# Kernel tuning notes

Hardware: AMD Instinct MI355X
Metric: run time of the kernel (lower is better)

The kernel has to match this reference:

```python
import jax, jax.numpy as jnp
import numpy as np

B, S, E, H, D = 2, 4096, 512, 8, 64  # batch, seq, embed, heads, key_dim


def setup_inputs() -> dict:
    key = jax.random.key(0)
    ks = jax.random.split(key, 8)
    queries = jax.random.normal(ks[0], (B, S, E), dtype=jnp.float32)
    keys = jax.random.normal(ks[1], (B, S, E), dtype=jnp.float32)
    values = jax.random.normal(ks[2], (B, S, E), dtype=jnp.float32)
    mask = jax.random.randint(ks[3], (B, H, S, S), 0, 2).astype(bool)
    scale = 1.0 / np.sqrt(E)
    Wq = jax.random.normal(ks[4], (E, H * D), dtype=jnp.float32) * scale
    Wk = jax.random.normal(ks[5], (E, H * D), dtype=jnp.float32) * scale
    Wv = jax.random.normal(ks[6], (E, H * D), dtype=jnp.float32) * scale
    Wo = jax.random.normal(ks[7], (H * D, E), dtype=jnp.float32) * scale
    return {"queries": queries, "keys": keys, "values": values, "mask": mask,
            "Wq": Wq, "Wk": Wk, "Wv": Wv, "Wo": Wo}


def reference(queries, keys, values, mask, Wq, Wk, Wv, Wo):
    # QKV projections (no bias), reshape to heads: (B, S, H, D)
    q = (queries @ Wq).reshape(B, -1, H, D)
    k = (keys @ Wk).reshape(B, -1, H, D)
    v = (values @ Wv).reshape(B, -1, H, D)
    # scores: (B, H, Sq, Sk)
    scores = jnp.einsum("bqhd,bkhd->bhqk", q, k) / jnp.sqrt(jnp.float32(D))
    scores = jnp.where(mask, jnp.float32(-1e10), scores)
    attn = jax.nn.softmax(scores, axis=-1)
    out = jnp.einsum("bhqk,bkhd->bqhd", attn, v).reshape(B, -1, H * D)
    return out @ Wo
```

## Files before the change

kernel.cpp:

```cpp
#include <hip/hip_runtime.h>
#include <hip/hip_bf16.h>

#define NB 2
#define NS 4096
#define NE 512
#define NH 8
#define ND 64
#define NHD 512

typedef __attribute__((ext_vector_type(8))) short short8;
typedef __attribute__((ext_vector_type(4))) float floatx4;
typedef __attribute__((ext_vector_type(16))) float f32x16;

#define MFMA16(a, b, c) __builtin_amdgcn_mfma_f32_16x16x32_bf16((a), (b), (c), 0, 0, 0)
#define MFMA32(a, b, c) __builtin_amdgcn_mfma_f32_32x32x16_bf16((a), (b), (c), 0, 0, 0)

union Cvt8 { uint4 u; short8 s; };
static __device__ __forceinline__ short8 ld8(const __hip_bfloat16* p) {
  Cvt8 c; c.u = *(const uint4*)p; return c.s;
}
union BH { __hip_bfloat16 h; short s; };
static __device__ __forceinline__ short f2bs(float x) {
  BH u; u.h = __float2bfloat16(x); return u.s;
}
static __device__ __forceinline__ unsigned pk2(float a, float b) {
  unsigned d;
  asm("v_cvt_pk_bf16_f32 %0, %1, %2" : "=v"(d) : "v"(a), "v"(b));
  return d;
}
static __device__ __forceinline__ float fexp2(float x) {
  float r;
  asm("v_exp_f32 %0, %1" : "=v"(r) : "v"(x));
  return r;
}

__global__ __launch_bounds__(256) void wconv(
    const float* w0, const float* w1, const float* w2, const float* w3,
    __hip_bfloat16* t0, __hip_bfloat16* t1,
    __hip_bfloat16* t2, __hip_bfloat16* t3) {
  __shared__ __hip_bfloat16 tile[64][72];
  const float* src;
  __hip_bfloat16* dst;
  switch (blockIdx.z) {
    case 0: src = w0; dst = t0; break;
    case 1: src = w1; dst = t1; break;
    case 2: src = w2; dst = t2; break;
    default: src = w3; dst = t3; break;
  }
  const int tx = threadIdx.x & 63, ty = threadIdx.x >> 6;
  const int n0 = blockIdx.x * 64, k0 = blockIdx.y * 64;
  for (int r = ty; r < 64; r += 4)
    tile[r][tx] = __float2bfloat16(src[(long)(k0 + r) * 512 + n0 + tx]);
  __syncthreads();
  for (int r = ty; r < 64; r += 4)
    dst[(long)(n0 + r) * 512 + k0 + tx] = tile[tx][r];
}

__global__ __launch_bounds__(256) void gemm_qkv(
    const float* A0, const float* A1, const float* A2,
    const __hip_bfloat16* W0, const __hip_bfloat16* W1, const __hip_bfloat16* W2,
    __hip_bfloat16* O0, __hip_bfloat16* O1, __hip_bfloat16* O2) {
  const float* A;
  const __hip_bfloat16* Wt;
  __hip_bfloat16* O;
  switch (blockIdx.z) {
    case 0: A = A0; Wt = W0; O = O0; break;
    case 1: A = A1; Wt = W1; O = O1; break;
    default: A = A2; Wt = W2; O = O2; break;
  }
  const int lane = threadIdx.x & 63;
  const int w = threadIdx.x >> 6;
  const int c = lane & 15, g = lane >> 4;
  const int m0 = blockIdx.x * 64 + w * 16;
  const int n0 = blockIdx.y * 64;

  floatx4 acc[4] = {};
  const float* ap = A + (long)(m0 + c) * 512 + g * 8;
  const __hip_bfloat16* wp = Wt + (long)(n0 + c) * 512 + g * 8;
  for (int ks = 0; ks < 512; ks += 32) {
    const float4 f0 = *(const float4*)(ap + ks);
    const float4 f1 = *(const float4*)(ap + ks + 4);
    short8 a;
    a[0] = f2bs(f0.x); a[1] = f2bs(f0.y); a[2] = f2bs(f0.z); a[3] = f2bs(f0.w);
    a[4] = f2bs(f1.x); a[5] = f2bs(f1.y); a[6] = f2bs(f1.z); a[7] = f2bs(f1.w);
#pragma unroll
    for (int t = 0; t < 4; ++t) {
      short8 b = ld8(wp + t * 16 * 512 + ks);
      acc[t] = MFMA16(a, b, acc[t]);
    }
  }
  const float sc = (blockIdx.z == 0) ? 0.125f * 1.44269504f : 1.0f;
#pragma unroll
  for (int t = 0; t < 4; ++t) {
#pragma unroll
    for (int r = 0; r < 4; ++r) {
      const int m = m0 + g * 4 + r;
      const int n = n0 + t * 16 + c;
      const int bb = m >> 12, s = m & 4095, h = n >> 6, d = n & 63;
      O[(((long)bb * NH + h) * NS + s) * ND + d] = __float2bfloat16(acc[t][r] * sc);
    }
  }
}

#define VPAD 72
__device__ __forceinline__ int vswz(int row) { return ((row >> 3) & 7) * 8; }

__global__ __launch_bounds__(256) void flash_attn(
    const __hip_bfloat16* Q, const __hip_bfloat16* K, const __hip_bfloat16* V,
    const int* __restrict__ mask, __hip_bfloat16* AO) {
  __shared__ __hip_bfloat16 Ks[64 * VPAD];
  __shared__ __hip_bfloat16 Vt[64 * VPAD];

  const int tid = threadIdx.x;
  const int lane = tid & 63, w = tid >> 6;
  const int ql = lane & 31, hl = lane >> 5;
  const int bz = blockIdx.z, hy = blockIdx.y;
  const int q0 = blockIdx.x * 128 + w * 32;
  const long headbase = ((long)bz * NH + hy) * NS;

  short8 qf[4];
#pragma unroll
  for (int ds = 0; ds < 4; ++ds)
    qf[ds] = ld8(Q + (headbase + q0 + ql) * ND + ds * 16 + hl * 8);

  f32x16 oacc0 = {}, oacc1 = {};
  float m_i = -1e30f, l_i = 0.f;
  const int* mrow = mask + (headbase + q0 + ql) * (long)NS;

  for (int kt = 0; kt < 64; ++kt) {
    const int k0 = kt * 64;

    int4 mk0, mk1, mk2, mk3, mk4, mk5, mk6, mk7;
    {
      const int* mp = mrow + k0 + 4 * hl;
      mk0 = *(const int4*)(mp + 0);
      mk1 = *(const int4*)(mp + 8);
      mk2 = *(const int4*)(mp + 16);
      mk3 = *(const int4*)(mp + 24);
      mk4 = *(const int4*)(mp + 32);
      mk5 = *(const int4*)(mp + 40);
      mk6 = *(const int4*)(mp + 48);
      mk7 = *(const int4*)(mp + 56);
    }

#pragma unroll
    for (int it = 0; it < 2; ++it) {
      const int chunk = tid + it * 256;
      const int kc = chunk >> 3;
      const int dd = (chunk & 7) * 8;
      const long gbase = (headbase + k0 + kc) * ND + dd;
      *(uint4*)&Ks[kc * VPAD + dd] = *(const uint4*)(K + gbase);
      uint4 vv = *(const uint4*)(V + gbase);
      const __hip_bfloat16* ve = (const __hip_bfloat16*)&vv;
#pragma unroll
      for (int j = 0; j < 8; ++j) {
        const int row = dd + j;
        Vt[row * VPAD + (kc ^ vswz(row))] = ve[j];
      }
    }
    __syncthreads();

    f32x16 s0 = {}, s1 = {};
#pragma unroll
    for (int ds = 0; ds < 4; ++ds) {
      short8 a0 = ld8(&Ks[ql * VPAD + ds * 16 + hl * 8]);
      s0 = MFMA32(a0, qf[ds], s0);
      short8 a1 = ld8(&Ks[(32 + ql) * VPAD + ds * 16 + hl * 8]);
      s1 = MFMA32(a1, qf[ds], s1);
    }

#pragma unroll
    for (int rr = 0; rr < 4; ++rr) {
      int4 a, b;
      switch (rr) {
        case 0: a = mk0; b = mk4; break;
        case 1: a = mk1; b = mk5; break;
        case 2: a = mk2; b = mk6; break;
        default: a = mk3; b = mk7; break;
      }
      if (a.x != 0) s0[4 * rr + 0] = -1e10f;
      if (a.y != 0) s0[4 * rr + 1] = -1e10f;
      if (a.z != 0) s0[4 * rr + 2] = -1e10f;
      if (a.w != 0) s0[4 * rr + 3] = -1e10f;
      if (b.x != 0) s1[4 * rr + 0] = -1e10f;
      if (b.y != 0) s1[4 * rr + 1] = -1e10f;
      if (b.z != 0) s1[4 * rr + 2] = -1e10f;
      if (b.w != 0) s1[4 * rr + 3] = -1e10f;
    }

    float mt = -1e30f;
#pragma unroll
    for (int r = 0; r < 16; ++r)
      mt = fmaxf(mt, fmaxf(s0[r], s1[r]));
    mt = fmaxf(mt, __shfl_xor(mt, 32));

    if (__ballot(mt > m_i + 8.0f) != 0ull) {
      const float mn = fmaxf(m_i, mt);
      const float al = fexp2(m_i - mn);
      m_i = mn;
      l_i *= al;
#pragma unroll
      for (int r = 0; r < 16; ++r) {
        const float ab = __shfl(al, (r & 3) + 8 * (r >> 2) + 4 * hl);
        oacc0[r] *= ab;
        oacc1[r] *= ab;
      }
    }

    float ss = 0.f;
#pragma unroll
    for (int r = 0; r < 16; ++r) {
      const float p0 = fexp2(s0[r] - m_i);
      const float p1 = fexp2(s1[r] - m_i);
      s0[r] = p0; s1[r] = p1;
      ss += p0 + p1;
    }
    ss += __shfl_xor(ss, 32);
    l_i += ss;

#pragma unroll
    for (int ks = 0; ks < 4; ++ks) {
      float pp[8];
#pragma unroll
      for (int j = 0; j < 8; ++j)
        pp[j] = (ks < 2) ? ((ks & 1) ? s0[8 + j] : s0[j])
                         : ((ks & 1) ? s1[8 + j] : s1[j]);
      const unsigned pk01 = pk2(pp[0], pp[1]);
      const unsigned pk23 = pk2(pp[2], pp[3]);
      const unsigned pk45 = pk2(pp[4], pp[5]);
      const unsigned pk67 = pk2(pp[6], pp[7]);
      const unsigned send1 = hl ? pk01 : pk45;
      const unsigned send2 = hl ? pk23 : pk67;
      const unsigned recv1 = __shfl_xor(send1, 32);
      const unsigned recv2 = __shfl_xor(send2, 32);
      Cvt8 pc;
      pc.u = make_uint4(hl ? recv1 : pk01,
                        hl ? recv2 : pk23,
                        hl ? pk45 : recv1,
                        hl ? pk67 : recv2);
      const int cb = ks * 16 + hl * 8;
      const short8 v0 = ld8(&Vt[ql * VPAD + (cb ^ vswz(ql))]);
      oacc0 = MFMA32(pc.s, v0, oacc0);
      const short8 v1 = ld8(&Vt[(32 + ql) * VPAD + (cb ^ vswz(32 + ql))]);
      oacc1 = MFMA32(pc.s, v1, oacc1);
    }
    __syncthreads();
  }

#pragma unroll
  for (int r = 0; r < 16; ++r) {
    const int cr = (r & 3) + 8 * (r >> 2) + 4 * hl;
    const float lb = __shfl(l_i, cr);
    const float inv = 1.0f / lb;
    const long obase = ((long)bz * NS + q0 + cr) * NHD + hy * 64;
    AO[obase + ql] = __float2bfloat16(oacc0[r] * inv);
    AO[obase + 32 + ql] = __float2bfloat16(oacc1[r] * inv);
  }
}

__global__ __launch_bounds__(256) void gemm_out(
    const __hip_bfloat16* A, const __hip_bfloat16* Wt, float* O) {
  const int lane = threadIdx.x & 63;
  const int w = threadIdx.x >> 6;
  const int c = lane & 15, g = lane >> 4;
  const int m0 = blockIdx.x * 64 + w * 16;
  const int n0 = blockIdx.y * 64;

  floatx4 acc[4] = {};
  const __hip_bfloat16* ap = A + (long)(m0 + c) * 512 + g * 8;
  const __hip_bfloat16* wp = Wt + (long)(n0 + c) * 512 + g * 8;
  for (int ks = 0; ks < 512; ks += 32) {
    short8 a = ld8(ap + ks);
#pragma unroll
    for (int t = 0; t < 4; ++t) {
      short8 b = ld8(wp + t * 16 * 512 + ks);
      acc[t] = MFMA16(a, b, acc[t]);
    }
  }
#pragma unroll
  for (int t = 0; t < 4; ++t)
#pragma unroll
    for (int r = 0; r < 4; ++r)
      O[(long)(m0 + g * 4 + r) * 512 + n0 + t * 16 + c] = acc[t][r];
}

extern "C" void kernel_launch(void* const* d_in, const int* in_sizes, int n_in,
                              void* d_out, int out_size, void* d_ws, size_t ws_size,
                              hipStream_t stream) {
  const float* q_in = (const float*)d_in[0];
  const float* k_in = (const float*)d_in[1];
  const float* v_in = (const float*)d_in[2];
  const int* mask = (const int*)d_in[3];
  const float* Wq = (const float*)d_in[4];
  const float* Wk = (const float*)d_in[5];
  const float* Wv = (const float*)d_in[6];
  const float* Wo = (const float*)d_in[7];
  float* out = (float*)d_out;

  char* base = (char*)d_ws;
  const size_t MB = 1u << 20;
  __hip_bfloat16* wtq = (__hip_bfloat16*)(base);
  __hip_bfloat16* wtk = (__hip_bfloat16*)(base + 512 * 1024);
  __hip_bfloat16* wtv = (__hip_bfloat16*)(base + 1 * MB);
  __hip_bfloat16* wto = (__hip_bfloat16*)(base + 1 * MB + 512 * 1024);
  __hip_bfloat16* qp = (__hip_bfloat16*)(base + 2 * MB);
  __hip_bfloat16* kp = (__hip_bfloat16*)(base + 10 * MB);
  __hip_bfloat16* vp = (__hip_bfloat16*)(base + 18 * MB);
  __hip_bfloat16* ao = (__hip_bfloat16*)(base + 26 * MB);

  wconv<<<dim3(8, 8, 4), 256, 0, stream>>>(Wq, Wk, Wv, Wo, wtq, wtk, wtv, wto);
  gemm_qkv<<<dim3(128, 8, 3), 256, 0, stream>>>(
      q_in, k_in, v_in, wtq, wtk, wtv, qp, kp, vp);
  flash_attn<<<dim3(NS / 128, NH, NB), 256, 0, stream>>>(qp, kp, vp, mask, ao);
  gemm_out<<<dim3(128, 8), 256, 0, stream>>>(ao, wto, out);
}
```

Before: 1.610 ms.

## Double-buffer K/V tiles with register prefetch and remap blocks across XCDs

Double-buffers the K and transposed-V tiles in shared memory. The next tile's global loads are issued into registers before this tile's compute and written to the other buffer afterwards, so one barrier per iteration remains and load latency is hidden behind the MFMAs. The mask is read with nontemporal loads, MFMA sections get raised wave priority, and the block index is remapped so blocks sharing a head land on the same XCD for L2 reuse. Costs are twice the LDS and more live registers, which may lower occupancy.

After: 1.689 ms. 4.9% more time.

```diff
diff --git a/kernel.cpp b/kernel.cpp
--- a/kernel.cpp
+++ b/kernel.cpp
@@ -11,6 +11,7 @@
 typedef __attribute__((ext_vector_type(8))) short short8;
 typedef __attribute__((ext_vector_type(4))) float floatx4;
 typedef __attribute__((ext_vector_type(16))) float f32x16;
+typedef __attribute__((ext_vector_type(4))) int intx4;
 
 #define MFMA16(a, b, c) __builtin_amdgcn_mfma_f32_16x16x32_bf16((a), (b), (c), 0, 0, 0)
 #define MFMA32(a, b, c) __builtin_amdgcn_mfma_f32_32x32x16_bf16((a), (b), (c), 0, 0, 0)
@@ -105,18 +106,52 @@
 #define VPAD 72
 __device__ __forceinline__ int vswz(int row) { return ((row >> 3) & 7) * 8; }
 
+#define STAGE_LOAD(kt_)                                                      \
+  do {                                                                       \
+    const long gb0 = (headbase + (kt_) * 64 + kc) * (long)ND + dd;           \
+    const long gb1 = gb0 + 32 * ND;                                          \
+    k0r = *(const uint4*)(K + gb0);                                          \
+    v0r = *(const uint4*)(V + gb0);                                          \
+    k1r = *(const uint4*)(K + gb1);                                          \
+    v1r = *(const uint4*)(V + gb1);                                          \
+  } while (0)
+
+#define STAGE_WRITE(buf_)                                                    \
+  do {                                                                       \
+    *(uint4*)&Ks[buf_][kc * VPAD + dd] = k0r;                                \
+    *(uint4*)&Ks[buf_][(kc + 32) * VPAD + dd] = k1r;                         \
+    const __hip_bfloat16* ve0 = (const __hip_bfloat16*)&v0r;                 \
+    const __hip_bfloat16* ve1 = (const __hip_bfloat16*)&v1r;                 \
+    _Pragma("unroll")                                                        \
+    for (int jj = 0; jj < 8; ++jj) {                                         \
+      const int row = dd + jj;                                               \
+      Vt[buf_][row * VPAD + (kc ^ vswz(row))] = ve0[jj];                     \
+      Vt[buf_][row * VPAD + ((kc + 32) ^ vswz(row))] = ve1[jj];              \
+    }                                                                        \
+  } while (0)
+
 __global__ __launch_bounds__(256) void flash_attn(
     const __hip_bfloat16* Q, const __hip_bfloat16* K, const __hip_bfloat16* V,
     const int* __restrict__ mask, __hip_bfloat16* AO) {
-  __shared__ __hip_bfloat16 Ks[64 * VPAD];
-  __shared__ __hip_bfloat16 Vt[64 * VPAD];
+  __shared__ __hip_bfloat16 Ks[2][64 * VPAD];
+  __shared__ __hip_bfloat16 Vt[2][64 * VPAD];
 
   const int tid = threadIdx.x;
   const int lane = tid & 63, w = tid >> 6;
   const int ql = lane & 31, hl = lane >> 5;
-  const int bz = blockIdx.z, hy = blockIdx.y;
-  const int q0 = blockIdx.x * 128 + w * 32;
+
+  const int L = blockIdx.x + 32 * (blockIdx.y + 8 * blockIdx.z);
+  const int cxcd = L & 7, j = L >> 3;
+  const int h2 = cxcd + 8 * (j >> 5);
+  const int bx = j & 31;
+  const int hy = h2 & 7, bz = h2 >> 3;
+
+  const int q0 = bx * 128 + w * 32;
   const long headbase = ((long)bz * NH + hy) * NS;
+
+  const int kc = tid >> 3;
+  const int dd = (tid & 7) * 8;
+  uint4 k0r, k1r, v0r, v1r;
 
   short8 qf[4];
 #pragma unroll
@@ -127,65 +162,45 @@
   float m_i = -1e30f, l_i = 0.f;
   const int* mrow = mask + (headbase + q0 + ql) * (long)NS;
 
+  STAGE_LOAD(0);
+  STAGE_WRITE(0);
+  __syncthreads();
+
   for (int kt = 0; kt < 64; ++kt) {
-    const int k0 = kt * 64;
-
-    int4 mk0, mk1, mk2, mk3, mk4, mk5, mk6, mk7;
+    const int cur = kt & 1;
+
+    intx4 mk[8];
     {
-      const int* mp = mrow + k0 + 4 * hl;
-      mk0 = *(const int4*)(mp + 0);
-      mk1 = *(const int4*)(mp + 8);
-      mk2 = *(const int4*)(mp + 16);
-      mk3 = *(const int4*)(mp + 24);
-      mk4 = *(const int4*)(mp + 32);
-      mk5 = *(const int4*)(mp + 40);
-      mk6 = *(const int4*)(mp + 48);
-      mk7 = *(const int4*)(mp + 56);
-    }
-
-#pragma unroll
-    for (int it = 0; it < 2; ++it) {
-      const int chunk = tid + it * 256;
-      const int kc = chunk >> 3;
-      const int dd = (chunk & 7) * 8;
-      const long gbase = (headbase + k0 + kc) * ND + dd;
-      *(uint4*)&Ks[kc * VPAD + dd] = *(const uint4*)(K + gbase);
-      uint4 vv = *(const uint4*)(V + gbase);
-      const __hip_bfloat16* ve = (const __hip_bfloat16*)&vv;
-#pragma unroll
-      for (int j = 0; j < 8; ++j) {
-        const int row = dd + j;
-        Vt[row * VPAD + (kc ^ vswz(row))] = ve[j];
-      }
-    }
-    __syncthreads();
+      const intx4* mp = (const intx4*)(mrow + kt * 64 + 4 * hl);
+#pragma unroll
+      for (int i = 0; i < 8; ++i)
+        mk[i] = __builtin_nontemporal_load(mp + 2 * i);
+    }
+
+    if (kt < 63) STAGE_LOAD(kt + 1);
 
     f32x16 s0 = {}, s1 = {};
+    __builtin_amdgcn_s_setprio(1);
 #pragma unroll
     for (int ds = 0; ds < 4; ++ds) {
-      short8 a0 = ld8(&Ks[ql * VPAD + ds * 16 + hl * 8]);
+      short8 a0 = ld8(&Ks[cur][ql * VPAD + ds * 16 + hl * 8]);
       s0 = MFMA32(a0, qf[ds], s0);
-      short8 a1 = ld8(&Ks[(32 + ql) * VPAD + ds * 16 + hl * 8]);
+      short8 a1 = ld8(&Ks[cur][(32 + ql) * VPAD + ds * 16 + hl * 8]);
       s1 = MFMA32(a1, qf[ds], s1);
     }
+    __builtin_amdgcn_s_setprio(0);
 
 #pragma unroll
     for (int rr = 0; rr < 4; ++rr) {
-      int4 a, b;
-      switch (rr) {
-        case 0: a = mk0; b = mk4; break;
-        case 1: a = mk1; b = mk5; break;
-        case 2: a = mk2; b = mk6; break;
-        default: a = mk3; b = mk7; break;
-      }
-      if (a.x != 0) s0[4 * rr + 0] = -1e10f;
-      if (a.y != 0) s0[4 * rr + 1] = -1e10f;
-      if (a.z != 0) s0[4 * rr + 2] = -1e10f;
-      if (a.w != 0) s0[4 * rr + 3] = -1e10f;
-      if (b.x != 0) s1[4 * rr + 0] = -1e10f;
-      if (b.y != 0) s1[4 * rr + 1] = -1e10f;
-      if (b.z != 0) s1[4 * rr + 2] = -1e10f;
-      if (b.w != 0) s1[4 * rr + 3] = -1e10f;
+      const intx4 a = mk[rr], b = mk[rr + 4];
+      if (a[0] != 0) s0[4 * rr + 0] = -1e10f;
+      if (a[1] != 0) s0[4 * rr + 1] = -1e10f;
+      if (a[2] != 0) s0[4 * rr + 2] = -1e10f;
+      if (a[3] != 0) s0[4 * rr + 3] = -1e10f;
+      if (b[0] != 0) s1[4 * rr + 0] = -1e10f;
+      if (b[1] != 0) s1[4 * rr + 1] = -1e10f;
+      if (b[2] != 0) s1[4 * rr + 2] = -1e10f;
+      if (b[3] != 0) s1[4 * rr + 3] = -1e10f;
     }
 
     float mt = -1e30f;
@@ -218,13 +233,14 @@
     ss += __shfl_xor(ss, 32);
     l_i += ss;
 
+    __builtin_amdgcn_s_setprio(1);
 #pragma unroll
     for (int ks = 0; ks < 4; ++ks) {
       float pp[8];
 #pragma unroll
-      for (int j = 0; j < 8; ++j)
-        pp[j] = (ks < 2) ? ((ks & 1) ? s0[8 + j] : s0[j])
-                         : ((ks & 1) ? s1[8 + j] : s1[j]);
+      for (int j2 = 0; j2 < 8; ++j2)
+        pp[j2] = (ks < 2) ? ((ks & 1) ? s0[8 + j2] : s0[j2])
+                          : ((ks & 1) ? s1[8 + j2] : s1[j2]);
       const unsigned pk01 = pk2(pp[0], pp[1]);
       const unsigned pk23 = pk2(pp[2], pp[3]);
       const unsigned pk45 = pk2(pp[4], pp[5]);
@@ -239,11 +255,14 @@
                         hl ? pk45 : recv1,
                         hl ? pk67 : recv2);
       const int cb = ks * 16 + hl * 8;
-      const short8 v0 = ld8(&Vt[ql * VPAD + (cb ^ vswz(ql))]);
+      const short8 v0 = ld8(&Vt[cur][ql * VPAD + (cb ^ vswz(ql))]);
       oacc0 = MFMA32(pc.s, v0, oacc0);
-      const short8 v1 = ld8(&Vt[(32 + ql) * VPAD + (cb ^ vswz(32 + ql))]);
+      const short8 v1 = ld8(&Vt[cur][(32 + ql) * VPAD + (cb ^ vswz(32 + ql))]);
       oacc1 = MFMA32(pc.s, v1, oacc1);
     }
+    __builtin_amdgcn_s_setprio(0);
+
+    if (kt < 63) STAGE_WRITE(cur ^ 1);
     __syncthreads();
   }
 
```
